# Kernel optimization log

Hardware: AMD Instinct MI355X
Metric: run time of the kernel (lower is better)

## Reference

```python
import math
import jax, jax.numpy as jnp
import numpy as np

B, T, D, H, HD, FF = 2, 2048, 768, 12, 64, 3072


def setup_inputs() -> dict:
    key = jax.random.key(0)
    ks = jax.random.split(key, 9)
    s = 0.02  # init scale
    x = jax.random.normal(ks[0], (B, T, D), jnp.float32)
    wq = jax.random.normal(ks[1], (D, D), jnp.float32) * s
    wk = jax.random.normal(ks[2], (D, D), jnp.float32) * s
    wv = jax.random.normal(ks[3], (D, D), jnp.float32) * s
    wo = jax.random.normal(ks[4], (D, D), jnp.float32) * s
    w1 = jax.random.normal(ks[5], (FF, D), jnp.float32) * s
    w2 = jax.random.normal(ks[6], (FF, D), jnp.float32) * s
    w3 = jax.random.normal(ks[7], (D, FF), jnp.float32) * s
    attn_norm_w = jnp.ones((D,), jnp.float32)
    ffn_norm_w = jnp.ones((D,), jnp.float32)
    # interleaved RoPE cache: values pair-repeated along head_dim
    inv_freq = 1.0 / (10000.0 ** (np.arange(0, HD, 2, dtype=np.float32) / HD))
    freqs = np.arange(T, dtype=np.float32)[:, None] * inv_freq[None, :]  # [T, HD/2]
    emb = np.repeat(freqs, 2, axis=-1)  # [T, HD]
    cos = jnp.asarray(np.cos(emb), jnp.float32)[None, None]  # [1,1,T,HD]
    sin = jnp.asarray(np.sin(emb), jnp.float32)[None, None]
    return {"x": x, "wq": wq, "wk": wk, "wv": wv, "wo": wo,
            "w1": w1, "w2": w2, "w3": w3,
            "attn_norm_w": attn_norm_w, "ffn_norm_w": ffn_norm_w,
            "cos": cos, "sin": sin}


def _rmsnorm(x, w, eps=1e-6):
    n = jnp.linalg.norm(x, axis=-1, keepdims=True)
    return w * x / (n / math.sqrt(x.shape[-1]) + eps)


def _rotate_half(x):
    x1, x2 = x[..., ::2], x[..., 1::2]
    return jnp.stack((-x2, x1), axis=-1).reshape(x.shape)


def _attention(x, wq, wk, wv, wo, cos, sin):
    b, t, c = x.shape
    q = (x @ wq.T).reshape(b, t, H, HD).transpose(0, 2, 1, 3)  # [B,H,T,hd]
    k = (x @ wk.T).reshape(b, t, H, HD).transpose(0, 2, 1, 3)
    v = (x @ wv.T).reshape(b, t, H, HD).transpose(0, 2, 1, 3)
    c_, s_ = cos[:, :, :t, :], sin[:, :, :t, :]
    q = q * c_ + _rotate_half(q) * s_
    k = k * c_ + _rotate_half(k) * s_
    att = jnp.einsum('bhqd,bhkd->bhqk', q, k) / math.sqrt(HD)
    mask = jnp.triu(jnp.full((t, t), -jnp.inf, att.dtype), k=1)
    att = jax.nn.softmax(att + mask, axis=-1)
    y = jnp.einsum('bhqk,bhkd->bhqd', att, v)
    y = y.transpose(0, 2, 1, 3).reshape(b, t, c)
    return y @ wo.T


def reference(x, wq, wk, wv, wo, w1, w2, w3, attn_norm_w, ffn_norm_w, cos, sin):
    x = x + _attention(_rmsnorm(x, attn_norm_w), wq, wk, wv, wo, cos, sin)
    h = _rmsnorm(x, ffn_norm_w)
    ff = (jax.nn.silu(h @ w1.T) * (h @ w2.T)) @ w3.T
    return x + ff
```

## Files before the change

kernel.cpp:

```cpp
#include <hip/hip_runtime.h>
#include <hip/hip_bf16.h>
#include <math.h>

typedef __bf16 bf16;
typedef __bf16 bf16x4 __attribute__((ext_vector_type(4)));
typedef __bf16 bf16x8 __attribute__((ext_vector_type(8)));
typedef float floatx4 __attribute__((ext_vector_type(4)));

#define T_ 2048
#define D_ 768
#define H_ 12
#define HD_ 64
#define FF_ 3072
#define LOG2E 1.44269504f
#define LDP 72

__device__ __forceinline__ floatx4 mfma_bf16(bf16x8 a, bf16x8 b, floatx4 c) {
  return __builtin_amdgcn_mfma_f32_16x16x32_bf16(a, b, c, 0, 0, 0);
}

__device__ __forceinline__ void rms_row(const float* __restrict__ x,
                                        const float* __restrict__ wt,
                                        bf16* __restrict__ o, int row, int tid) {
  const long off = (long)row * D_;
  float vals[3];
  float ss = 0.f;
#pragma unroll
  for (int i = 0; i < 3; i++) {
    vals[i] = x[off + tid + i * 256];
    ss += vals[i] * vals[i];
  }
#pragma unroll
  for (int d = 1; d < 64; d <<= 1) ss += __shfl_xor(ss, d);
  __shared__ float wsum[4];
  if ((tid & 63) == 0) wsum[tid >> 6] = ss;
  __syncthreads();
  const float tot = wsum[0] + wsum[1] + wsum[2] + wsum[3];
  const float inv = 1.0f / (sqrtf(tot * (1.0f / 768.0f)) + 1e-6f);
#pragma unroll
  for (int i = 0; i < 3; i++)
    o[off + tid + i * 256] = (bf16)(vals[i] * inv * wt[tid + i * 256]);
}

__global__ __launch_bounds__(256)
void prep_k(const float* __restrict__ wq, const float* __restrict__ wk,
            const float* __restrict__ wv, const float* __restrict__ wo,
            const float* __restrict__ w1, const float* __restrict__ w2,
            const float* __restrict__ w3, bf16* __restrict__ o,
            const float* __restrict__ x, const float* __restrict__ anw,
            bf16* __restrict__ hn) {
  if (blockIdx.x >= 4608) {
    rms_row(x, anw, hn, blockIdx.x - 4608, threadIdx.x);
    return;
  }
  const long i = ((long)blockIdx.x * 256 + threadIdx.x) * 8;
  const float* s;
  if      (i <  589824) s = wq + i;
  else if (i < 1179648) s = wk + (i -  589824);
  else if (i < 1769472) s = wv + (i - 1179648);
  else if (i < 2359296) s = wo + (i - 1769472);
  else if (i < 4718592) s = w1 + (i - 2359296);
  else if (i < 7077888) s = w2 + (i - 4718592);
  else                  s = w3 + (i - 7077888);
  const floatx4 a = *(const floatx4*)s;
  const floatx4 b = *(const floatx4*)(s + 4);
  bf16x8 r;
#pragma unroll
  for (int j = 0; j < 4; j++) { r[j] = (bf16)a[j]; r[4 + j] = (bf16)b[j]; }
  *(bf16x8*)&o[i] = r;
}

__global__ __launch_bounds__(256)
void rmsnorm_k(const float* __restrict__ x, const float* __restrict__ wt,
               bf16* __restrict__ o) {
  rms_row(x, wt, o, blockIdx.x, threadIdx.x);
}

__global__ __launch_bounds__(256)
void gemm_qkv(const bf16* __restrict__ A, const bf16* __restrict__ wq,
              const bf16* __restrict__ wk, const bf16* __restrict__ wv,
              bf16* __restrict__ q, bf16* __restrict__ k, bf16* __restrict__ vt,
              const float* __restrict__ cosb, const float* __restrict__ sinb) {
  const int widx = blockIdx.x / 6;
  const int nb   = blockIdx.x % 6;
  const bf16* W = (widx == 0) ? wq : (widx == 1) ? wk : wv;
  const int m0 = blockIdx.y * 128, n0 = nb * 128;
  const int K = D_;

  __shared__ __align__(16) bf16 As[128 * LDP];
  __shared__ __align__(16) bf16 Ws[128 * LDP];

  const int tid = threadIdx.x;
  const int lane = tid & 63;
  const int wm = tid >> 7;
  const int wn = (tid >> 6) & 1;
  const int fr = lane & 15;
  const int fk = (lane >> 4) * 8;

  floatx4 acc[4][4] = {};

  const int ar = tid >> 3;
  const int ac = (tid & 7) * 8;
  const bf16* Aptr = A + (long)(m0 + ar) * K + ac;
  const bf16* Wptr = W + (long)(n0 + ar) * K + ac;
  const long rstep = (long)32 * K;

  bf16x8 apf[4], wpf[4];
#pragma unroll
  for (int c = 0; c < 4; c++) apf[c] = *(const bf16x8*)(Aptr + c * rstep);
#pragma unroll
  for (int c = 0; c < 4; c++) wpf[c] = *(const bf16x8*)(Wptr + c * rstep);

  const int ns = K >> 6;
  for (int ks = 0; ks < ns; ks++) {
    __syncthreads();
#pragma unroll
    for (int c = 0; c < 4; c++) *(bf16x8*)&As[(ar + c * 32) * LDP + ac] = apf[c];
#pragma unroll
    for (int c = 0; c < 4; c++) *(bf16x8*)&Ws[(ar + c * 32) * LDP + ac] = wpf[c];
    __syncthreads();
    const long koff = (long)((ks + 1 < ns) ? ks + 1 : ks) * 64;
#pragma unroll
    for (int c = 0; c < 4; c++) apf[c] = *(const bf16x8*)(Aptr + koff + c * rstep);
#pragma unroll
    for (int c = 0; c < 4; c++) wpf[c] = *(const bf16x8*)(Wptr + koff + c * rstep);
#pragma unroll
    for (int kc = 0; kc < 2; kc++) {
      bf16x8 af[4], bfv[4];
#pragma unroll
      for (int i = 0; i < 4; i++) af[i]  = *(const bf16x8*)&As[(wm * 64 + i * 16 + fr) * LDP + kc * 32 + fk];
#pragma unroll
      for (int j = 0; j < 4; j++) bfv[j] = *(const bf16x8*)&Ws[(wn * 64 + j * 16 + fr) * LDP + kc * 32 + fk];
#pragma unroll
      for (int i = 0; i < 4; i++)
#pragma unroll
        for (int j = 0; j < 4; j++)
          acc[i][j] = mfma_bf16(af[i], bfv[j], acc[i][j]);
    }
  }

  const int rb = (lane >> 4) * 4;
  if (widx < 2) {
    bf16* O = (widx == 0) ? q : k;
    const float sgn = (fr & 1) ? 1.f : -1.f;
#pragma unroll
    for (int i = 0; i < 4; i++)
#pragma unroll
      for (int j = 0; j < 4; j++) {
        const int n = n0 + wn * 64 + j * 16 + fr;
        const int d = n & 63;
#pragma unroll
        for (int r = 0; r < 4; r++) {
          const int m = m0 + wm * 64 + i * 16 + rb + r;
          const int pos = m & (T_ - 1);
          const float val = acc[i][j][r];
          const float par = __shfl_xor(val, 1);
          const float cc = cosb[pos * HD_ + d];
          const float ss = sinb[pos * HD_ + d];
          O[(long)m * D_ + n] = (bf16)(val * cc + sgn * par * ss);
        }
      }
  } else {
#pragma unroll
    for (int i = 0; i < 4; i++)
#pragma unroll
      for (int j = 0; j < 4; j++) {
        const int n = n0 + wn * 64 + j * 16 + fr;
        const int m = m0 + wm * 64 + i * 16 + rb;
        const int b = m >> 11;
        const int t = m & (T_ - 1);
        const long row = (long)(b * H_ + (n >> 6)) * HD_ + (n & 63);
        bf16x4 pk;
#pragma unroll
        for (int r = 0; r < 4; r++) pk[r] = (bf16)acc[i][j][r];
        *(bf16x4*)&vt[row * T_ + t] = pk;
      }
  }
}

__global__ __launch_bounds__(256)
void gemm_n64(const bf16* __restrict__ A, const bf16* __restrict__ W,
              float* __restrict__ C, const float* __restrict__ resid,
              int N, int K) {
  __shared__ __align__(16) bf16 As[128 * LDP];
  __shared__ __align__(16) bf16 Ws[64 * LDP];

  const int L  = blockIdx.x;
  const int j  = L >> 3;
  const int mb = (L & 7) * 4 + (j / 12);
  const int nb = j % 12;
  const int m0 = mb * 128, n0 = nb * 64;

  const int tid = threadIdx.x;
  const int lane = tid & 63;
  const int wm = tid >> 7;
  const int wn = (tid >> 6) & 1;
  const int fr = lane & 15;
  const int fk = (lane >> 4) * 8;

  floatx4 acc[4][2] = {};

  const int ar = tid >> 3;
  const int ac = (tid & 7) * 8;
  const bf16* Aptr = A + (long)(m0 + ar) * K + ac;
  const bf16* Wptr = W + (long)(n0 + ar) * K + ac;
  const long rstep = (long)32 * K;

  bf16x8 apf[4], wpf[2];
#pragma unroll
  for (int c = 0; c < 4; c++) apf[c] = *(const bf16x8*)(Aptr + c * rstep);
#pragma unroll
  for (int c = 0; c < 2; c++) wpf[c] = *(const bf16x8*)(Wptr + c * rstep);

  const int ns = K >> 6;
  for (int ks = 0; ks < ns; ks++) {
    __syncthreads();
#pragma unroll
    for (int c = 0; c < 4; c++) *(bf16x8*)&As[(ar + c * 32) * LDP + ac] = apf[c];
#pragma unroll
    for (int c = 0; c < 2; c++) *(bf16x8*)&Ws[(ar + c * 32) * LDP + ac] = wpf[c];
    __syncthreads();
    const long koff = (long)((ks + 1 < ns) ? ks + 1 : ks) * 64;
#pragma unroll
    for (int c = 0; c < 4; c++) apf[c] = *(const bf16x8*)(Aptr + koff + c * rstep);
#pragma unroll
    for (int c = 0; c < 2; c++) wpf[c] = *(const bf16x8*)(Wptr + koff + c * rstep);
#pragma unroll
    for (int kc = 0; kc < 2; kc++) {
      bf16x8 af[4], bfv[2];
#pragma unroll
      for (int i = 0; i < 4; i++) af[i]  = *(const bf16x8*)&As[(wm * 64 + i * 16 + fr) * LDP + kc * 32 + fk];
#pragma unroll
      for (int j2 = 0; j2 < 2; j2++) bfv[j2] = *(const bf16x8*)&Ws[(wn * 32 + j2 * 16 + fr) * LDP + kc * 32 + fk];
#pragma unroll
      for (int i = 0; i < 4; i++)
#pragma unroll
        for (int j2 = 0; j2 < 2; j2++)
          acc[i][j2] = mfma_bf16(af[i], bfv[j2], acc[i][j2]);
    }
  }

  const int rb = (lane >> 4) * 4;
#pragma unroll
  for (int i = 0; i < 4; i++)
#pragma unroll
    for (int j2 = 0; j2 < 2; j2++) {
      const int n = n0 + wn * 32 + j2 * 16 + fr;
#pragma unroll
      for (int r = 0; r < 4; r++) {
        const int m = m0 + wm * 64 + i * 16 + rb + r;
        const long idx = (long)m * N + n;
        C[idx] = acc[i][j2][r] + resid[idx];
      }
    }
}

__global__ __launch_bounds__(256)
void gemm_w3sk(const bf16* __restrict__ A, const bf16* __restrict__ W,
               float* __restrict__ p0, float* __restrict__ p1) {
  __shared__ __align__(16) bf16 As[128 * LDP];
  __shared__ __align__(16) bf16 Ws[64 * LDP];

  const int L  = blockIdx.x;
  const int j  = L >> 3;
  const int mb = (L & 7) * 4 + (j / 24);
  const int inner = j % 24;
  const int s  = inner / 12;
  const int nb = inner % 12;
  const int m0 = mb * 128, n0 = nb * 64;
  const int K = FF_;
  const int kbase = s * 1536;
  float* C = s ? p1 : p0;

  const int tid = threadIdx.x;
  const int lane = tid & 63;
  const int wm = tid >> 7;
  const int wn = (tid >> 6) & 1;
  const int fr = lane & 15;
  const int fk = (lane >> 4) * 8;

  floatx4 acc[4][2] = {};

  const int ar = tid >> 3;
  const int ac = (tid & 7) * 8;
  const bf16* Aptr = A + (long)(m0 + ar) * K + kbase + ac;
  const bf16* Wptr = W + (long)(n0 + ar) * K + kbase + ac;
  const long rstep = (long)32 * K;

  bf16x8 apf[4], wpf[2];
#pragma unroll
  for (int c = 0; c < 4; c++) apf[c] = *(const bf16x8*)(Aptr + c * rstep);
#pragma unroll
  for (int c = 0; c < 2; c++) wpf[c] = *(const bf16x8*)(Wptr + c * rstep);

  const int ns = 24;
  for (int ks = 0; ks < ns; ks++) {
    __syncthreads();
#pragma unroll
    for (int c = 0; c < 4; c++) *(bf16x8*)&As[(ar + c * 32) * LDP + ac] = apf[c];
#pragma unroll
    for (int c = 0; c < 2; c++) *(bf16x8*)&Ws[(ar + c * 32) * LDP + ac] = wpf[c];
    __syncthreads();
    const long koff = (long)((ks + 1 < ns) ? ks + 1 : ks) * 64;
#pragma unroll
    for (int c = 0; c < 4; c++) apf[c] = *(const bf16x8*)(Aptr + koff + c * rstep);
#pragma unroll
    for (int c = 0; c < 2; c++) wpf[c] = *(const bf16x8*)(Wptr + koff + c * rstep);
#pragma unroll
    for (int kc = 0; kc < 2; kc++) {
      bf16x8 af[4], bfv[2];
#pragma unroll
      for (int i = 0; i < 4; i++) af[i]  = *(const bf16x8*)&As[(wm * 64 + i * 16 + fr) * LDP + kc * 32 + fk];
#pragma unroll
      for (int j2 = 0; j2 < 2; j2++) bfv[j2] = *(const bf16x8*)&Ws[(wn * 32 + j2 * 16 + fr) * LDP + kc * 32 + fk];
#pragma unroll
      for (int i = 0; i < 4; i++)
#pragma unroll
        for (int j2 = 0; j2 < 2; j2++)
          acc[i][j2] = mfma_bf16(af[i], bfv[j2], acc[i][j2]);
    }
  }

  const int rb = (lane >> 4) * 4;
#pragma unroll
  for (int i = 0; i < 4; i++)
#pragma unroll
    for (int j2 = 0; j2 < 2; j2++) {
      const int n = n0 + wn * 32 + j2 * 16 + fr;
#pragma unroll
      for (int r = 0; r < 4; r++) {
        const int m = m0 + wm * 64 + i * 16 + rb + r;
        C[(long)m * D_ + n] = acc[i][j2][r];
      }
    }
}

__global__ __launch_bounds__(256)
void comb3_k(const float* __restrict__ p0, const float* __restrict__ p1,
             const float* __restrict__ xm, float* __restrict__ out) {
  const long i = ((long)blockIdx.x * 256 + threadIdx.x) * 8;
#pragma unroll
  for (int c = 0; c < 2; c++) {
    const floatx4 a = *(const floatx4*)&p0[i + c * 4];
    const floatx4 b = *(const floatx4*)&p1[i + c * 4];
    const floatx4 d = *(const floatx4*)&xm[i + c * 4];
    floatx4 r;
#pragma unroll
    for (int e = 0; e < 4; e++) r[e] = a[e] + b[e] + d[e];
    *(floatx4*)&out[i + c * 4] = r;
  }
}

__global__ __launch_bounds__(256, 2)
void gemm_w12(const bf16* __restrict__ A, const bf16* __restrict__ W1,
              const bf16* __restrict__ W2, bf16* __restrict__ G) {
  __shared__ __align__(16) bf16 As[128 * LDP];
  __shared__ __align__(16) bf16 W1s[128 * LDP];
  __shared__ __align__(16) bf16 W2s[128 * LDP];

  const int L  = blockIdx.x;
  const int j  = L >> 3;
  const int mb = j / 3;
  const int nb = (L & 7) * 3 + (j % 3);
  const int m0 = mb * 128, n0 = nb * 128;
  const int K = D_;

  const int tid = threadIdx.x;
  const int lane = tid & 63;
  const int wm = tid >> 7;
  const int wn = (tid >> 6) & 1;
  const int fr = lane & 15;
  const int fk = (lane >> 4) * 8;

  floatx4 acc1[4][4] = {}, acc2[4][4] = {};

  const int ar = tid >> 3;
  const int ac = (tid & 7) * 8;
  const bf16* Aptr  = A  + (long)(m0 + ar) * K + ac;
  const bf16* W1ptr = W1 + (long)(n0 + ar) * K + ac;
  const bf16* W2ptr = W2 + (long)(n0 + ar) * K + ac;
  const long rstep = (long)32 * K;

  bf16x8 apf[4], w1pf[4], w2pf[4];
#pragma unroll
  for (int c = 0; c < 4; c++) { apf[c]  = *(const bf16x8*)(Aptr  + c * rstep);
                                w1pf[c] = *(const bf16x8*)(W1ptr + c * rstep);
                                w2pf[c] = *(const bf16x8*)(W2ptr + c * rstep); }

  const int ns = K >> 6;
  for (int ks = 0; ks < ns; ks++) {
    __syncthreads();
#pragma unroll
    for (int c = 0; c < 4; c++) { *(bf16x8*)&As[(ar + c * 32) * LDP + ac]  = apf[c];
                                  *(bf16x8*)&W1s[(ar + c * 32) * LDP + ac] = w1pf[c];
                                  *(bf16x8*)&W2s[(ar + c * 32) * LDP + ac] = w2pf[c]; }
    __syncthreads();
    const long koff = (long)((ks + 1 < ns) ? ks + 1 : ks) * 64;
#pragma unroll
    for (int c = 0; c < 4; c++) { apf[c]  = *(const bf16x8*)(Aptr  + koff + c * rstep);
                                  w1pf[c] = *(const bf16x8*)(W1ptr + koff + c * rstep);
                                  w2pf[c] = *(const bf16x8*)(W2ptr + koff + c * rstep); }
#pragma unroll
    for (int kc = 0; kc < 2; kc++) {
      bf16x8 af[4];
#pragma unroll
      for (int i = 0; i < 4; i++) af[i] = *(const bf16x8*)&As[(wm * 64 + i * 16 + fr) * LDP + kc * 32 + fk];
      {
        bf16x8 b1[4];
#pragma unroll
        for (int jj = 0; jj < 4; jj++) b1[jj] = *(const bf16x8*)&W1s[(wn * 64 + jj * 16 + fr) * LDP + kc * 32 + fk];
#pragma unroll
        for (int i = 0; i < 4; i++)
#pragma unroll
          for (int jj = 0; jj < 4; jj++)
            acc1[i][jj] = mfma_bf16(af[i], b1[jj], acc1[i][jj]);
      }
      {
        bf16x8 b2[4];
#pragma unroll
        for (int jj = 0; jj < 4; jj++) b2[jj] = *(const bf16x8*)&W2s[(wn * 64 + jj * 16 + fr) * LDP + kc * 32 + fk];
#pragma unroll
        for (int i = 0; i < 4; i++)
#pragma unroll
          for (int jj = 0; jj < 4; jj++)
            acc2[i][jj] = mfma_bf16(af[i], b2[jj], acc2[i][jj]);
      }
    }
  }

  const int rb = (lane >> 4) * 4;
#pragma unroll
  for (int i = 0; i < 4; i++)
#pragma unroll
    for (int jj = 0; jj < 4; jj++) {
      const int n = n0 + wn * 64 + jj * 16 + fr;
#pragma unroll
      for (int r = 0; r < 4; r++) {
        const int m = m0 + wm * 64 + i * 16 + rb + r;
        const float a1 = acc1[i][jj][r];
        const float a2 = acc2[i][jj][r];
        const float s = a1 / (1.f + exp2f(-a1 * LOG2E));
        G[(long)m * FF_ + n] = (bf16)(s * a2);
      }
    }
}

__global__ __launch_bounds__(256, 4)
void flash_attn(const bf16* __restrict__ q, const bf16* __restrict__ k,
                const bf16* __restrict__ vtg, float* __restrict__ po,
                float* __restrict__ pm, float* __restrict__ pl) {
  const int gid = blockIdx.x;
  const int bh = gid % 24;
  const int r  = gid / 24;
  int qt, c;
  if (r < 8)       { qt = r; c = 0; }
  else if (r < 24) { qt = 8 + ((r - 8) >> 1); c = (r - 8) & 1; }
  else if (r < 48) { const int u = r - 24; const int d = u / 3; qt = 16 + d; c = u - d * 3; }
  else             { const int u = r - 48; qt = 24 + (u >> 2); c = u & 3; }
  const int b  = bh / H_;
  const int h  = bh % H_;
  const int q0 = qt * 64;
  const int tbeg = c * 8;
  const int tend = (tbeg + 7 < qt) ? tbeg + 7 : qt;

  __shared__ __align__(16) bf16 Qs[64][72];
  __shared__ __align__(16) bf16 Ks[64][72];
  __shared__ __align__(16) bf16 Vt[64][72];
  __shared__ __align__(16) bf16 Ps[4][16][72];

  const int tid = threadIdx.x, lane = tid & 63, w = tid >> 6;
  const int fr = lane & 15, quad = lane >> 4, fk = quad * 8;
  const long base = ((long)b * T_) * D_ + h * HD_;
  const long vbase = (long)bh * HD_ * T_;

  const int srow = tid >> 2, scol = (tid & 3) * 16;
  {
    const long g = base + (long)(q0 + srow) * D_ + scol;
    *(bf16x8*)&Qs[srow][scol]     = *(const bf16x8*)&q[g];
    *(bf16x8*)&Qs[srow][scol + 8] = *(const bf16x8*)&q[g + 8];
  }

  const bf16* kgp = k + base + (long)srow * D_ + scol;
  const bf16* vgp = vtg + vbase + (long)srow * T_ + scol;
  bf16x8 kpf0 = *(const bf16x8*)(kgp + (long)tbeg * 64 * D_);
  bf16x8 kpf1 = *(const bf16x8*)(kgp + (long)tbeg * 64 * D_ + 8);
  bf16x8 vpf0 = *(const bf16x8*)(vgp + tbeg * 64);
  bf16x8 vpf1 = *(const bf16x8*)(vgp + tbeg * 64 + 8);

  float m_st = -1e30f, l_st = 0.f;
  floatx4 o[4] = {};
  const float SC = 0.125f * LOG2E;

  for (int t = tbeg; t <= tend; t++) {
    __syncthreads();
    *(bf16x8*)&Ks[srow][scol]     = kpf0;
    *(bf16x8*)&Ks[srow][scol + 8] = kpf1;
    *(bf16x8*)&Vt[srow][scol]     = vpf0;
    *(bf16x8*)&Vt[srow][scol + 8] = vpf1;
    __syncthreads();
    const int tn = (t + 1 <= tend) ? t + 1 : t;
    kpf0 = *(const bf16x8*)(kgp + (long)tn * 64 * D_);
    kpf1 = *(const bf16x8*)(kgp + (long)tn * 64 * D_ + 8);
    vpf0 = *(const bf16x8*)(vgp + tn * 64);
    vpf1 = *(const bf16x8*)(vgp + tn * 64 + 8);

    floatx4 s[4] = {};
#pragma unroll
    for (int kd = 0; kd < 2; kd++) {
      const bf16x8 bq = *(const bf16x8*)&Qs[w * 16 + fr][kd * 32 + fk];
#pragma unroll
      for (int kt = 0; kt < 4; kt++) {
        const bf16x8 ak = *(const bf16x8*)&Ks[kt * 16 + fr][kd * 32 + fk];
        s[kt] = mfma_bf16(ak, bq, s[kt]);
      }
    }

    if (t == qt) {
      const int qloc = w * 16 + fr;
#pragma unroll
      for (int kt = 0; kt < 4; kt++)
#pragma unroll
        for (int r2 = 0; r2 < 4; r2++) {
          const int kvloc = kt * 16 + quad * 4 + r2;
          s[kt][r2] = (kvloc > qloc) ? -1e30f : s[kt][r2] * SC;
        }
    } else {
#pragma unroll
      for (int kt = 0; kt < 4; kt++)
#pragma unroll
        for (int r2 = 0; r2 < 4; r2++) s[kt][r2] *= SC;
    }

    float mx = -1e30f;
#pragma unroll
    for (int kt = 0; kt < 4; kt++)
#pragma unroll
      for (int r2 = 0; r2 < 4; r2++) mx = fmaxf(mx, s[kt][r2]);
    mx = fmaxf(mx, __shfl_xor(mx, 16));
    mx = fmaxf(mx, __shfl_xor(mx, 32));
    const float mnew  = fmaxf(m_st, mx);
    const float alpha = exp2f(m_st - mnew);
    m_st = mnew;
    float rs = 0.f;
#pragma unroll
    for (int kt = 0; kt < 4; kt++)
#pragma unroll
      for (int r2 = 0; r2 < 4; r2++) {
        const float pv = exp2f(s[kt][r2] - mnew);
        s[kt][r2] = pv;
        rs += pv;
      }
    rs += __shfl_xor(rs, 16);
    rs += __shfl_xor(rs, 32);
    l_st = l_st * alpha + rs;
#pragma unroll
    for (int ht = 0; ht < 4; ht++) o[ht] *= alpha;

#pragma unroll
    for (int kt = 0; kt < 4; kt++) {
      bf16x4 pk;
#pragma unroll
      for (int r2 = 0; r2 < 4; r2++) pk[r2] = (bf16)s[kt][r2];
      *(bf16x4*)&Ps[w][fr][kt * 16 + quad * 4] = pk;
    }

#pragma unroll
    for (int kq = 0; kq < 2; kq++) {
      const bf16x8 bp = *(const bf16x8*)&Ps[w][fr][kq * 32 + fk];
#pragma unroll
      for (int ht = 0; ht < 4; ht++) {
        const bf16x8 av = *(const bf16x8*)&Vt[ht * 16 + fr][kq * 32 + fk];
        o[ht] = mfma_bf16(av, bp, o[ht]);
      }
    }
  }

  const int qq = w * 16 + fr;
  const long pg = (long)gid * 4096 + qq * 64;
#pragma unroll
  for (int ht = 0; ht < 4; ht++)
    *(floatx4*)&po[pg + ht * 16 + quad * 4] = o[ht];
  if (quad == 0) { pm[gid * 64 + qq] = m_st; pl[gid * 64 + qq] = l_st; }
}

__global__ __launch_bounds__(256)
void flash_comb(const float* __restrict__ po, const float* __restrict__ pm,
                const float* __restrict__ pl, bf16* __restrict__ y) {
  const int bh = blockIdx.x >> 5;
  const int qt = blockIdx.x & 31;
  const int b = bh / H_, h = bh % H_;
  const int nc = (qt >> 3) + 1;
  int bse;
  if      (qt <  8) bse = qt;
  else if (qt < 16) bse = 8  + 2 * (qt - 8);
  else if (qt < 24) bse = 24 + 3 * (qt - 16);
  else              bse = 48 + 4 * (qt - 24);

  const int t = threadIdx.x;
  const int qq = t >> 2, hg = (t & 3) * 16;

  float M = -1e30f;
  for (int c2 = 0; c2 < nc; c2++) M = fmaxf(M, pm[((bse + c2) * 24 + bh) * 64 + qq]);
  float l = 0.f;
  floatx4 o[4] = {};
  for (int c2 = 0; c2 < nc; c2++) {
    const int g = (bse + c2) * 24 + bh;
    const float wgt = exp2f(pm[g * 64 + qq] - M);
    l += wgt * pl[g * 64 + qq];
    const long pg = (long)g * 4096 + qq * 64 + hg;
#pragma unroll
    for (int j = 0; j < 4; j++) {
      const floatx4 t4 = *(const floatx4*)&po[pg + j * 4];
#pragma unroll
      for (int e = 0; e < 4; e++) o[j][e] += wgt * t4[e];
    }
  }
  const float inv = 1.f / l;
  bf16x8 r0, r1;
#pragma unroll
  for (int e = 0; e < 4; e++) {
    r0[e]     = (bf16)(o[0][e] * inv);
    r0[4 + e] = (bf16)(o[1][e] * inv);
    r1[e]     = (bf16)(o[2][e] * inv);
    r1[4 + e] = (bf16)(o[3][e] * inv);
  }
  const long yoff = ((long)b * T_ + qt * 64 + qq) * D_ + h * HD_ + hg;
  *(bf16x8*)&y[yoff]     = r0;
  *(bf16x8*)&y[yoff + 8] = r1;
}

extern "C" void kernel_launch(void* const* d_in, const int* in_sizes, int n_in,
                              void* d_out, int out_size, void* d_ws, size_t ws_size,
                              hipStream_t stream) {
  const float* x    = (const float*)d_in[0];
  const float* wq   = (const float*)d_in[1];
  const float* wk   = (const float*)d_in[2];
  const float* wv   = (const float*)d_in[3];
  const float* wo   = (const float*)d_in[4];
  const float* w1   = (const float*)d_in[5];
  const float* w2   = (const float*)d_in[6];
  const float* w3   = (const float*)d_in[7];
  const float* anw  = (const float*)d_in[8];
  const float* fnw  = (const float*)d_in[9];
  const float* cosb = (const float*)d_in[10];
  const float* sinb = (const float*)d_in[11];

  char* ws = (char*)d_ws;
  bf16*  wb  = (bf16*)(ws + 0);
  bf16*  wqb = wb;
  bf16*  wkb = wb +  589824;
  bf16*  wvb = wb + 1179648;
  bf16*  wob = wb + 1769472;
  bf16*  w1b = wb + 2359296;
  bf16*  w2b = wb + 4718592;
  bf16*  w3b = wb + 7077888;
  bf16*  qb  = (bf16*)(ws + 18874368);
  bf16*  kb  = (bf16*)(ws + 25165824);
  bf16*  vt  = (bf16*)(ws + 31457280);
  bf16*  yb  = (bf16*)(ws + 37748736);
  bf16*  hn  = (bf16*)(ws + 44040192);
  float* xm  = (float*)(ws + 50331648);
  bf16*  g   = (bf16*)(ws + 62914560);
  float* po  = (float*)(ws + 50331648);
  float* pm  = (float*)(ws + 81788928);
  float* pl  = (float*)(ws + 82280448);
  float* p30 = (float*)(ws + 18874368);
  float* p31 = (float*)(ws + 37748736);

  prep_k<<<8704, 256, 0, stream>>>(wq, wk, wv, wo, w1, w2, w3, wb, x, anw, hn);
  gemm_qkv<<<dim3(18, 32), 256, 0, stream>>>(hn, wqb, wkb, wvb, qb, kb, vt, cosb, sinb);
  flash_attn<<<1920, 256, 0, stream>>>(qb, kb, vt, po, pm, pl);
  flash_comb<<<768, 256, 0, stream>>>(po, pm, pl, yb);
  gemm_n64<<<384, 256, 0, stream>>>(yb, wob, xm, x, 768, 768);
  rmsnorm_k<<<4096, 256, 0, stream>>>(xm, fnw, hn);
  gemm_w12<<<768, 256, 0, stream>>>(hn, w1b, w2b, g);
  gemm_w3sk<<<768, 256, 0, stream>>>(g, w3b, p30, p31);
  comb3_k<<<1536, 256, 0, stream>>>(p30, p31, xm, (float*)d_out);
}
```

Measured before the change: 293.1 us.

## Split W3 GEMM K three ways and stream W1/W2 fragments directly from global

```diff
diff --git a/kernel.cpp b/kernel.cpp
--- a/kernel.cpp
+++ b/kernel.cpp
@@ -257,20 +257,21 @@
 
 __global__ __launch_bounds__(256)
 void gemm_w3sk(const bf16* __restrict__ A, const bf16* __restrict__ W,
-               float* __restrict__ p0, float* __restrict__ p1) {
+               float* __restrict__ p0, float* __restrict__ p1,
+               float* __restrict__ p2) {
   __shared__ __align__(16) bf16 As[128 * LDP];
   __shared__ __align__(16) bf16 Ws[64 * LDP];
 
   const int L  = blockIdx.x;
   const int j  = L >> 3;
-  const int mb = (L & 7) * 4 + (j / 24);
-  const int inner = j % 24;
+  const int mb = (L & 7) * 4 + (j / 36);
+  const int inner = j % 36;
   const int s  = inner / 12;
   const int nb = inner % 12;
   const int m0 = mb * 128, n0 = nb * 64;
   const int K = FF_;
-  const int kbase = s * 1536;
-  float* C = s ? p1 : p0;
+  const int kbase = s * 1024;
+  float* C = (s == 0) ? p0 : (s == 1) ? p1 : p2;
 
   const int tid = threadIdx.x;
   const int lane = tid & 63;
@@ -293,7 +294,7 @@
 #pragma unroll
   for (int c = 0; c < 2; c++) wpf[c] = *(const bf16x8*)(Wptr + c * rstep);
 
-  const int ns = 24;
+  const int ns = 16;
   for (int ks = 0; ks < ns; ks++) {
     __syncthreads();
 #pragma unroll
@@ -337,26 +338,26 @@
 
 __global__ __launch_bounds__(256)
 void comb3_k(const float* __restrict__ p0, const float* __restrict__ p1,
-             const float* __restrict__ xm, float* __restrict__ out) {
+             const float* __restrict__ p2, const float* __restrict__ xm,
+             float* __restrict__ out) {
   const long i = ((long)blockIdx.x * 256 + threadIdx.x) * 8;
 #pragma unroll
   for (int c = 0; c < 2; c++) {
     const floatx4 a = *(const floatx4*)&p0[i + c * 4];
     const floatx4 b = *(const floatx4*)&p1[i + c * 4];
+    const floatx4 e = *(const floatx4*)&p2[i + c * 4];
     const floatx4 d = *(const floatx4*)&xm[i + c * 4];
     floatx4 r;
 #pragma unroll
-    for (int e = 0; e < 4; e++) r[e] = a[e] + b[e] + d[e];
+    for (int q = 0; q < 4; q++) r[q] = a[q] + b[q] + e[q] + d[q];
     *(floatx4*)&out[i + c * 4] = r;
   }
 }
 
-__global__ __launch_bounds__(256, 2)
+__global__ __launch_bounds__(256)
 void gemm_w12(const bf16* __restrict__ A, const bf16* __restrict__ W1,
               const bf16* __restrict__ W2, bf16* __restrict__ G) {
   __shared__ __align__(16) bf16 As[128 * LDP];
-  __shared__ __align__(16) bf16 W1s[128 * LDP];
-  __shared__ __align__(16) bf16 W2s[128 * LDP];
 
   const int L  = blockIdx.x;
   const int j  = L >> 3;
@@ -376,55 +377,46 @@
 
   const int ar = tid >> 3;
   const int ac = (tid & 7) * 8;
-  const bf16* Aptr  = A  + (long)(m0 + ar) * K + ac;
-  const bf16* W1ptr = W1 + (long)(n0 + ar) * K + ac;
-  const bf16* W2ptr = W2 + (long)(n0 + ar) * K + ac;
+  const bf16* Aptr = A + (long)(m0 + ar) * K + ac;
   const long rstep = (long)32 * K;
 
-  bf16x8 apf[4], w1pf[4], w2pf[4];
-#pragma unroll
-  for (int c = 0; c < 4; c++) { apf[c]  = *(const bf16x8*)(Aptr  + c * rstep);
-                                w1pf[c] = *(const bf16x8*)(W1ptr + c * rstep);
-                                w2pf[c] = *(const bf16x8*)(W2ptr + c * rstep); }
+  const bf16* W1p = W1 + (long)(n0 + wn * 64 + fr) * K + fk;
+  const bf16* W2p = W2 + (long)(n0 + wn * 64 + fr) * K + fk;
+  const long nstep = (long)16 * K;
+
+  bf16x8 apf[4];
+#pragma unroll
+  for (int c = 0; c < 4; c++) apf[c] = *(const bf16x8*)(Aptr + c * rstep);
 
   const int ns = K >> 6;
   for (int ks = 0; ks < ns; ks++) {
     __syncthreads();
 #pragma unroll
-    for (int c = 0; c < 4; c++) { *(bf16x8*)&As[(ar + c * 32) * LDP + ac]  = apf[c];
-                                  *(bf16x8*)&W1s[(ar + c * 32) * LDP + ac] = w1pf[c];
-                                  *(bf16x8*)&W2s[(ar + c * 32) * LDP + ac] = w2pf[c]; }
+    for (int c = 0; c < 4; c++) *(bf16x8*)&As[(ar + c * 32) * LDP + ac] = apf[c];
     __syncthreads();
     const long koff = (long)((ks + 1 < ns) ? ks + 1 : ks) * 64;
 #pragma unroll
-    for (int c = 0; c < 4; c++) { apf[c]  = *(const bf16x8*)(Aptr  + koff + c * rstep);
-                                  w1pf[c] = *(const bf16x8*)(W1ptr + koff + c * rstep);
-                                  w2pf[c] = *(const bf16x8*)(W2ptr + koff + c * rstep); }
+    for (int c = 0; c < 4; c++) apf[c] = *(const bf16x8*)(Aptr + koff + c * rstep);
 #pragma unroll
     for (int kc = 0; kc < 2; kc++) {
-      bf16x8 af[4];
+      const long kof = (long)ks * 64 + kc * 32;
+      bf16x8 b1[4], b2[4], af[4];
+#pragma unroll
+      for (int jj = 0; jj < 4; jj++) b1[jj] = *(const bf16x8*)(W1p + jj * nstep + kof);
+#pragma unroll
+      for (int jj = 0; jj < 4; jj++) b2[jj] = *(const bf16x8*)(W2p + jj * nstep + kof);
 #pragma unroll
       for (int i = 0; i < 4; i++) af[i] = *(const bf16x8*)&As[(wm * 64 + i * 16 + fr) * LDP + kc * 32 + fk];
-      {
-        bf16x8 b1[4];
-#pragma unroll
-        for (int jj = 0; jj < 4; jj++) b1[jj] = *(const bf16x8*)&W1s[(wn * 64 + jj * 16 + fr) * LDP + kc * 32 + fk];
-#pragma unroll
-        for (int i = 0; i < 4; i++)
-#pragma unroll
-          for (int jj = 0; jj < 4; jj++)
-            acc1[i][jj] = mfma_bf16(af[i], b1[jj], acc1[i][jj]);
-      }
-      {
-        bf16x8 b2[4];
-#pragma unroll
-        for (int jj = 0; jj < 4; jj++) b2[jj] = *(const bf16x8*)&W2s[(wn * 64 + jj * 16 + fr) * LDP + kc * 32 + fk];
-#pragma unroll
-        for (int i = 0; i < 4; i++)
-#pragma unroll
-          for (int jj = 0; jj < 4; jj++)
-            acc2[i][jj] = mfma_bf16(af[i], b2[jj], acc2[i][jj]);
-      }
+#pragma unroll
+      for (int i = 0; i < 4; i++)
+#pragma unroll
+        for (int jj = 0; jj < 4; jj++)
+          acc1[i][jj] = mfma_bf16(af[i], b1[jj], acc1[i][jj]);
+#pragma unroll
+      for (int i = 0; i < 4; i++)
+#pragma unroll
+        for (int jj = 0; jj < 4; jj++)
+          acc2[i][jj] = mfma_bf16(af[i], b2[jj], acc2[i][jj]);
     }
   }
 
@@ -664,8 +656,9 @@
   float* po  = (float*)(ws + 50331648);
   float* pm  = (float*)(ws + 81788928);
   float* pl  = (float*)(ws + 82280448);
-  float* p30 = (float*)(ws + 18874368);
-  float* p31 = (float*)(ws + 37748736);
+  float* pA  = (float*)(ws + 0);
+  float* pB  = (float*)(ws + 18874368);
+  float* pC  = (float*)(ws + 37748736);
 
   prep_k<<<8704, 256, 0, stream>>>(wq, wk, wv, wo, w1, w2, w3, wb, x, anw, hn);
   gemm_qkv<<<dim3(18, 32), 256, 0, stream>>>(hn, wqb, wkb, wvb, qb, kb, vt, cosb, sinb);
@@ -674,6 +667,6 @@
   gemm_n64<<<384, 256, 0, stream>>>(yb, wob, xm, x, 768, 768);
   rmsnorm_k<<<4096, 256, 0, stream>>>(xm, fnw, hn);
   gemm_w12<<<768, 256, 0, stream>>>(hn, w1b, w2b, g);
-  gemm_w3sk<<<768, 256, 0, stream>>>(g, w3b, p30, p31);
-  comb3_k<<<1536, 256, 0, stream>>>(p30, p31, xm, (float*)d_out);
-}
+  gemm_w3sk<<<1152, 256, 0, stream>>>(g, w3b, pA, pB, pC);
+  comb3_k<<<1536, 256, 0, stream>>>(pA, pB, pC, xm, (float*)d_out);
+}
```

Result: slower. 356.2 us (+21.5%).
